# Kernel optimization log

Measured on AMD Instinct MI355X. Metric: run time of the kernel, lower is better.

Reference implementation:

```python
import jax, jax.numpy as jnp
import numpy as np

T, B, D, H, L = 512, 128, 256, 256, 4
EPS = 1e-5

def _ln(x, g, b):
    m = jnp.mean(x, axis=-1, keepdims=True)
    v = jnp.mean((x - m) ** 2, axis=-1, keepdims=True)
    return (x - m) * jax.lax.rsqrt(v + EPS) * g + b

def setup_inputs() -> dict:
    key = jax.random.key(0)
    ks = jax.random.split(key, 24)
    s = 0.02
    inp = {
        "x": jax.random.normal(ks[0], (T, B, D), dtype=jnp.float32),
        "lengths": jax.random.randint(ks[1], (B,), 1, T + 1, dtype=jnp.int32),
        # LinearEnchancedGRU params
        "Wr": jax.random.normal(ks[2], (D + H, H)) * s,
        "gr": jnp.ones((H,)), "br": jnp.zeros((H,)),
        "Wz": jax.random.normal(ks[3], (D + H, H)) * s,
        "gz": jnp.ones((H,)), "bz": jnp.zeros((H,)),
        "Wl": jax.random.normal(ks[4], (D + H, H)) * s,
        "gl": jnp.ones((H,)), "bl": jnp.zeros((H,)),
        "Wlt": jax.random.normal(ks[5], (D, H)) * s,
        "Cx": jax.random.normal(ks[6], (D, H)) * s,
        "Ch_w": jax.random.normal(ks[7], (H, H)) * s,
        "Ch_b": jnp.zeros((H,)),
        # TransitionGRU stack params [L, ...]
        "tWr": jax.random.normal(ks[8], (L, H, H)) * s,
        "tgr": jnp.ones((L, H)), "tbr": jnp.zeros((L, H)),
        "tWz": jax.random.normal(ks[9], (L, H, H)) * s,
        "tgz": jnp.ones((L, H)), "tbz": jnp.zeros((L, H)),
        "tWc": jax.random.normal(ks[10], (L, H, H)) * s,
        "tbc": jnp.zeros((L, H)),
    }
    return inp

def reference(x, lengths, Wr, gr, br, Wz, gz, bz, Wl, gl, bl, Wlt, Cx, Ch_w, Ch_b,
              tWr, tgr, tbr, tWz, tgz, tbz, tWc, tbc):
    # x: [T,B,D]; lengths: [B]. Packed-sequence semantics: hidden state of a
    # finished example is frozen; its outputs are zero padding.
    mask = jnp.arange(T, dtype=jnp.int32)[:, None] < lengths[None, :]  # [T,B]

    def cell(xt, h):
        cat = jnp.concatenate([xt, h], axis=-1)  # [B, D+H]
        r = jax.nn.sigmoid(_ln(cat @ Wr, gr, br))
        z = jax.nn.sigmoid(_ln(cat @ Wz, gz, bz))
        l = jax.nn.sigmoid(_ln(cat @ Wl, gl, bl))
        n = jnp.tanh(xt @ Cx + r * (h @ Ch_w + Ch_b)) + l * (xt @ Wlt)
        h = (1.0 - z) * h + z * n
        for i in range(L):  # deep transition stack (fixed small depth)
            ri = jax.nn.sigmoid(_ln(h @ tWr[i], tgr[i], tbr[i]))
            zi = jax.nn.sigmoid(_ln(h @ tWz[i], tgz[i], tbz[i]))
            ni = jnp.tanh(ri * (h @ tWc[i] + tbc[i]))
            h = (1.0 - zi) * ni + zi * h
        return h

    def step(h, inputs):
        xt, mt = inputs  # [B,D], [B]
        hn = cell(xt, h)
        hn = jnp.where(mt[:, None], hn, h)
        out = jnp.where(mt[:, None], hn, 0.0)
        return hn, out

    h0 = jnp.zeros((B, H), dtype=x.dtype)
    _, outs = jax.lax.scan(step, h0, (x, mask))  # outs: [T,B,H]
    return outs
```

## Files before the change

### kernel.cpp

```cpp
#include <hip/hip_runtime.h>
#include <hip/hip_bf16.h>

#define T_ 512
#define B_ 128
#define D_ 256
#define H_ 256
#define EPS 1e-5f

typedef __attribute__((ext_vector_type(8))) short short8;
typedef __attribute__((ext_vector_type(4))) short short4v;
typedef __attribute__((ext_vector_type(4))) float f32x4;

#define SLICE_E  86016
#define WT_TOTAL 1376256

#define STATS_OFFB 2752512UL
#define HX_OFFB    2850816UL
#define FLAG_OFFB  2981888UL
#define NFLAGS     512

#define L_XBF  0
#define L_HBF  8192
#define L_G6   16384
#define L_SRED 22528
#define L_AUX  23040
#define L_TRN  47616
#define L_END  145920

__device__ __forceinline__ short f2bf(float f) {
  unsigned u = __builtin_bit_cast(unsigned, f);
  u = (u + 0x7FFFu + ((u >> 16) & 1u)) >> 16;
  return (short)u;
}
__device__ __forceinline__ f32x4 zero4() { f32x4 z = {0.f, 0.f, 0.f, 0.f}; return z; }
__device__ __forceinline__ f32x4 mfma16(short8 a, short8 b, f32x4 c) {
  return __builtin_amdgcn_mfma_f32_16x16x32_bf16(a, b, c, 0, 0, 0);
}
__device__ __forceinline__ void waitv0() { asm volatile("s_waitcnt vmcnt(0)" ::: "memory"); }

__device__ __forceinline__ f32x4 ald4(float* p) {
  unsigned long long* q = (unsigned long long*)p;
  unsigned long long a = __hip_atomic_load(q,     __ATOMIC_RELAXED, __HIP_MEMORY_SCOPE_AGENT);
  unsigned long long b = __hip_atomic_load(q + 1, __ATOMIC_RELAXED, __HIP_MEMORY_SCOPE_AGENT);
  f32x4 v;
  v[0] = __builtin_bit_cast(float, (unsigned)(a & 0xffffffffu));
  v[1] = __builtin_bit_cast(float, (unsigned)(a >> 32));
  v[2] = __builtin_bit_cast(float, (unsigned)(b & 0xffffffffu));
  v[3] = __builtin_bit_cast(float, (unsigned)(b >> 32));
  return v;
}
__device__ __forceinline__ void ast1f(float* p, float v) {
  __hip_atomic_store((unsigned*)p, __builtin_bit_cast(unsigned, v),
                     __ATOMIC_RELAXED, __HIP_MEMORY_SCOPE_AGENT);
}

__global__ void prep_weights(const float* __restrict__ Wr, const float* __restrict__ Wz,
                             const float* __restrict__ Wl, const float* __restrict__ Wlt,
                             const float* __restrict__ Cx, const float* __restrict__ Chw,
                             const float* __restrict__ tWr, const float* __restrict__ tWz,
                             const float* __restrict__ tWc, short* __restrict__ wt) {
  int idx = blockIdx.x * 256 + threadIdx.x;
  if (idx >= WT_TOTAL) return;
  int j  = idx / SLICE_E;
  int r  = idx - j * SLICE_E;
  int u  = r >> 12;
  int rr = r & 4095;
  int kf = rr >> 9;
  int le = rr & 511;
  int l  = le >> 3, e = le & 7;
  int la = l & 15, lh = l >> 4;
  int col = j * 16 + la;
  float v;
  if (u < 6) {
    int g = u >> 1, half = u & 1;
    int k = half * 256 + lh * 8 + kf * 32 + e;
    const float* W = (g == 0) ? Wr : (g == 1 ? Wz : Wl);
    v = W[k * 256 + col];
  } else if (u < 9) {
    int a = u - 6;
    int k = lh * 8 + kf * 32 + e;
    const float* W = (a == 0) ? Cx : (a == 1 ? Wlt : Chw);
    v = W[k * 256 + col];
  } else {
    int q = u - 9;
    int li = q / 3, m = q - li * 3;
    int k = lh * 8 + kf * 32 + e;
    const float* W = (m == 0) ? tWr : (m == 1 ? tWz : tWc);
    v = W[(li * 256 + k) * 256 + col];
  }
  wt[idx] = f2bf(v);
}

__global__ __launch_bounds__(64)
void rnn_sx(const float* __restrict__ x, const int* __restrict__ lengths,
            const float* __restrict__ gr, const float* __restrict__ br,
            const float* __restrict__ gz, const float* __restrict__ bz,
            const float* __restrict__ gl, const float* __restrict__ bl,
            const float* __restrict__ Chb,
            const float* __restrict__ tgr, const float* __restrict__ tbr,
            const float* __restrict__ tgz, const float* __restrict__ tbz,
            const float* __restrict__ tbc,
            const short* __restrict__ W, float* __restrict__ stats,
            short* __restrict__ hxs, unsigned* __restrict__ flags,
            float* __restrict__ out) {

  __shared__ __align__(16) char smem[L_END];

  const int l  = threadIdx.x;
  const int la = l & 15, lh = l >> 4;
  const int amask = (la & 7) << 4;
  const int bid = blockIdx.x;
  const int cl = bid & 7, j = bid >> 3;
  const int rb0 = cl * 16;
  const int myrow = l >> 2, mc = (l & 3) * 4;
  const int cg = j * 16 + mc;
  const int colb = (l & 3) * 64;

  const short* Wsl = W + (size_t)j * SLICE_E;

  #pragma unroll 1
  for (int u = 0; u < 15; ++u) {
    char* dst = smem + ((u < 3) ? (L_AUX + u * 8192) : (L_TRN + (u - 3) * 8192));
    const short* src = Wsl + (size_t)(u + 6) * 4096;
    #pragma unroll
    for (int kf = 0; kf < 8; ++kf)
      *(short8*)(dst + kf * 1024 + l * 16) = *(const short8*)(src + kf * 512 + l * 8);
  }
  for (int i = l; i < 1024; i += 64) ((short4v*)(smem + L_HBF))[i] = (short4v){0, 0, 0, 0};

  int maxlen = 0;
  for (int i = 0; i < 16; ++i) {
    int v = lengths[rb0 + i];
    maxlen = maxlen > v ? maxlen : v;
  }
  const int mylen = lengths[rb0 + myrow];

  float* stc = stats + (size_t)(cl * 2) * 1536;
  short* hxc = hxs + (size_t)(cl * 2) * 4096;
  unsigned* flc = flags + cl * 64;

  f32x4 hreg = zero4();
  int dead = 0;

  auto pollf = [&](unsigned* fb, unsigned tag) {
    if (!dead) {
      int it = 0;
      while (true) {
        unsigned v = tag;
        if (l < 16) v = __hip_atomic_load(fb + l, __ATOMIC_RELAXED, __HIP_MEMORY_SCOPE_AGENT);
        if (__all((int)(v >= tag))) break;
        if (++it > 300000) { dead = 1; break; }
        __builtin_amdgcn_s_sleep(1);
      }
    }
    asm volatile("" ::: "memory");
  };
  auto ldu = [&](short8 (&dst)[8], const short* bp) {
    #pragma unroll
    for (int kf = 0; kf < 8; ++kf) dst[kf] = *(const short8*)(bp + kf * 512 + l * 8);
  };
  auto mm8r = [&](short8 (&Bv)[8], f32x4& acc, int Ab) {
    #pragma unroll
    for (int kf = 0; kf < 8; ++kf) {
      int aoff = Ab + la * 512 + (((kf * 64) + lh * 16) ^ amask);
      acc = mfma16(*(const short8*)(smem + aoff), Bv[kf], acc);
    }
  };
  auto mmlds = [&](int Bub, f32x4& acc, int Ab) {
    #pragma unroll
    for (int kf = 0; kf < 8; ++kf) {
      int aoff = Ab + la * 512 + (((kf * 64) + lh * 16) ^ amask);
      short8 bv = *(const short8*)(smem + Bub + kf * 1024 + l * 16);
      acc = mfma16(*(const short8*)(smem + aoff), bv, acc);
    }
  };
  auto g6store = [&](int arr, f32x4 acc) {
    #pragma unroll
    for (int i = 0; i < 4; ++i)
      *(float*)(smem + L_G6 + ((arr * 16 + lh * 4 + i) * 16 + la) * 4) = acc[i];
  };
  auto readhx = [&](int par) {
    float* hp = (float*)(hxc + par * 4096 + (l >> 2) * 256 + colb);
    int row2 = l >> 2;
    #pragma unroll
    for (int q2 = 0; q2 < 8; ++q2) {
      f32x4 v = ald4(hp + q2 * 4);
      *(f32x4*)(smem + L_HBF + row2 * 512 + ((colb * 2 + q2 * 16) ^ ((row2 & 7) << 4))) = v;
    }
  };
  auto posth = [&](int par) {
    unsigned long long pk =
        (unsigned long long)(unsigned short)f2bf(hreg[0]) |
        ((unsigned long long)(unsigned short)f2bf(hreg[1]) << 16) |
        ((unsigned long long)(unsigned short)f2bf(hreg[2]) << 32) |
        ((unsigned long long)(unsigned short)f2bf(hreg[3]) << 48);
    __hip_atomic_store((unsigned long long*)(hxc + par * 4096 + myrow * 256 + cg), pk,
                       __ATOMIC_RELAXED, __HIP_MEMORY_SCOPE_AGENT);
  };

  short8 B0[8], B1[8];
  ldu(B0, Wsl);
  ldu(B1, Wsl + 4096);

  for (int t = 0; t < maxlen; ++t) {
    int R = t * 5, par = R & 1;
    {
      const float* xs = x + ((size_t)t * B_ + rb0 + (l >> 2)) * D_ + colb;
      int row2 = l >> 2;
      #pragma unroll
      for (int u2 = 0; u2 < 8; ++u2) {
        f32x4 a = *(const f32x4*)(xs + u2 * 8);
        f32x4 b = *(const f32x4*)(xs + u2 * 8 + 4);
        short8 s;
        s[0] = f2bf(a[0]); s[1] = f2bf(a[1]); s[2] = f2bf(a[2]); s[3] = f2bf(a[3]);
        s[4] = f2bf(b[0]); s[5] = f2bf(b[1]); s[6] = f2bf(b[2]); s[7] = f2bf(b[3]);
        *(short8*)(smem + L_XBF + row2 * 512 + ((colb * 2 + u2 * 16) ^ ((row2 & 7) << 4))) = s;
      }
    }
    f32x4 ac[6];
    #pragma unroll
    for (int a2 = 0; a2 < 6; ++a2) ac[a2] = zero4();
    mm8r(B0, ac[0], L_XBF); ldu(B0, Wsl + 2 * 4096);
    mm8r(B1, ac[0], L_HBF); ldu(B1, Wsl + 3 * 4096);
    mm8r(B0, ac[1], L_XBF); ldu(B0, Wsl + 4 * 4096);
    mm8r(B1, ac[1], L_HBF); ldu(B1, Wsl + 5 * 4096);
    mm8r(B0, ac[2], L_XBF);
    mm8r(B1, ac[2], L_HBF);
    mmlds(L_AUX,         ac[3], L_XBF);
    mmlds(L_AUX + 8192,  ac[4], L_XBF);
    mmlds(L_AUX + 16384, ac[5], L_HBF);
    #pragma unroll
    for (int a2 = 0; a2 < 6; ++a2) g6store(a2, ac[a2]);
    f32x4 pv[6];
    #pragma unroll
    for (int a2 = 0; a2 < 6; ++a2)
      pv[a2] = *(const f32x4*)(smem + L_G6 + ((a2 * 16 + myrow) * 16 + mc) * 4);
    float st[6];
    #pragma unroll
    for (int g2 = 0; g2 < 3; ++g2) {
      f32x4 v = pv[g2];
      st[2 * g2]     = v[0] + v[1] + v[2] + v[3];
      st[2 * g2 + 1] = v[0] * v[0] + v[1] * v[1] + v[2] * v[2] + v[3] * v[3];
    }
    #pragma unroll
    for (int s2 = 0; s2 < 6; ++s2) {
      st[s2] += __shfl_xor(st[s2], 1);
      st[s2] += __shfl_xor(st[s2], 2);
    }
    float* sp = stc + par * 1536;
    {
      int k4 = l & 3;
      ast1f(sp + (k4 * 16 + myrow) * 16 + j, st[k4]);
      if (k4 < 2) ast1f(sp + ((4 + k4) * 16 + myrow) * 16 + j, st[4 + k4]);
    }
    waitv0();
    if (l == 0)
      __hip_atomic_store(flc + par * 16 + j, (unsigned)(R + 1),
                         __ATOMIC_RELAXED, __HIP_MEMORY_SCOPE_AGENT);
    pollf(flc + par * 16, (unsigned)(R + 1));
    {
      float* q = sp + l * 16;
      f32x4 a = ald4(q), b = ald4(q + 4), c = ald4(q + 8), d = ald4(q + 12);
      f32x4 s4 = a + b + c + d;
      *(float*)(smem + L_SRED + l * 4) = s4[0] + s4[1] + s4[2] + s4[3];
      if (l < 32) {
        float* q2 = sp + (64 + l) * 16;
        f32x4 a2 = ald4(q2), b2 = ald4(q2 + 4), c2 = ald4(q2 + 8), d2 = ald4(q2 + 12);
        f32x4 t4 = a2 + b2 + c2 + d2;
        *(float*)(smem + L_SRED + (64 + l) * 4) = t4[0] + t4[1] + t4[2] + t4[3];
      }
    }
    {
      float m3[3], rs3[3];
      #pragma unroll
      for (int g2 = 0; g2 < 3; ++g2) {
        float s1 = *(float*)(smem + L_SRED + ((2 * g2) * 16 + myrow) * 4);
        float s2 = *(float*)(smem + L_SRED + ((2 * g2 + 1) * 16 + myrow) * 4);
        float mm = s1 * (1.f / 256.f);
        float vv = s2 * (1.f / 256.f) - mm * mm;
        m3[g2] = mm; rs3[g2] = rsqrtf((vv > 0.f ? vv : 0.f) + EPS);
      }
      f32x4 g4r = *(const f32x4*)(gr + cg), b4r = *(const f32x4*)(br + cg);
      f32x4 g4z = *(const f32x4*)(gz + cg), b4z = *(const f32x4*)(bz + cg);
      f32x4 g4l = *(const f32x4*)(gl + cg), b4l = *(const f32x4*)(bl + cg);
      f32x4 cb4 = *(const f32x4*)(Chb + cg);
      bool act = t < mylen;
      f32x4 hn;
      #pragma unroll
      for (int q2 = 0; q2 < 4; ++q2) {
        float rv = 1.f / (1.f + __expf(-((pv[0][q2] - m3[0]) * rs3[0] * g4r[q2] + b4r[q2])));
        float zv = 1.f / (1.f + __expf(-((pv[1][q2] - m3[1]) * rs3[1] * g4z[q2] + b4z[q2])));
        float lv = 1.f / (1.f + __expf(-((pv[2][q2] - m3[2]) * rs3[2] * g4l[q2] + b4l[q2])));
        float n = tanhf(pv[3][q2] + rv * (pv[5][q2] + cb4[q2])) + lv * pv[4][q2];
        hn[q2] = (1.f - zv) * hreg[q2] + zv * n;
      }
      if (act) hreg = hn;
    }
    posth(par);
    waitv0();
    if (l == 0)
      __hip_atomic_store(flc + (2 + par) * 16 + j, (unsigned)(R + 1),
                         __ATOMIC_RELAXED, __HIP_MEMORY_SCOPE_AGENT);
    pollf(flc + (2 + par) * 16, (unsigned)(R + 1));
    readhx(par);

    #pragma unroll 1
    for (int li = 0; li < 4; ++li) {
      R = t * 5 + 1 + li; par = R & 1;
      f32x4 tc0 = zero4(), tc1 = zero4(), tc2 = zero4();
      mmlds(L_TRN + (li * 3 + 0) * 8192, tc0, L_HBF);
      mmlds(L_TRN + (li * 3 + 1) * 8192, tc1, L_HBF);
      mmlds(L_TRN + (li * 3 + 2) * 8192, tc2, L_HBF);
      g6store(0, tc0); g6store(1, tc1); g6store(2, tc2);
      f32x4 qv[3];
      #pragma unroll
      for (int a2 = 0; a2 < 3; ++a2)
        qv[a2] = *(const f32x4*)(smem + L_G6 + ((a2 * 16 + myrow) * 16 + mc) * 4);
      float st4[4];
      #pragma unroll
      for (int g2 = 0; g2 < 2; ++g2) {
        f32x4 v = qv[g2];
        st4[2 * g2]     = v[0] + v[1] + v[2] + v[3];
        st4[2 * g2 + 1] = v[0] * v[0] + v[1] * v[1] + v[2] * v[2] + v[3] * v[3];
      }
      #pragma unroll
      for (int s2 = 0; s2 < 4; ++s2) {
        st4[s2] += __shfl_xor(st4[s2], 1);
        st4[s2] += __shfl_xor(st4[s2], 2);
      }
      float* sp2 = stc + par * 1536;
      ast1f(sp2 + ((l & 3) * 16 + myrow) * 16 + j, st4[l & 3]);
      waitv0();
      if (l == 0)
        __hip_atomic_store(flc + par * 16 + j, (unsigned)(R + 1),
                           __ATOMIC_RELAXED, __HIP_MEMORY_SCOPE_AGENT);
      if (li == 3) {
        ldu(B0, Wsl);
        ldu(B1, Wsl + 4096);
      }
      pollf(flc + par * 16, (unsigned)(R + 1));
      {
        float* q = sp2 + l * 16;
        f32x4 a = ald4(q), b = ald4(q + 4), c = ald4(q + 8), d = ald4(q + 12);
        f32x4 s4 = a + b + c + d;
        *(float*)(smem + L_SRED + l * 4) = s4[0] + s4[1] + s4[2] + s4[3];
      }
      bool act = t < mylen;
      {
        float m2[2], rs2[2];
        #pragma unroll
        for (int g2 = 0; g2 < 2; ++g2) {
          float s1 = *(float*)(smem + L_SRED + ((2 * g2) * 16 + myrow) * 4);
          float s2 = *(float*)(smem + L_SRED + ((2 * g2 + 1) * 16 + myrow) * 4);
          float mm = s1 * (1.f / 256.f);
          float vv = s2 * (1.f / 256.f) - mm * mm;
          m2[g2] = mm; rs2[g2] = rsqrtf((vv > 0.f ? vv : 0.f) + EPS);
        }
        f32x4 g4r = *(const f32x4*)(tgr + li * 256 + cg), b4r = *(const f32x4*)(tbr + li * 256 + cg);
        f32x4 g4z = *(const f32x4*)(tgz + li * 256 + cg), b4z = *(const f32x4*)(tbz + li * 256 + cg);
        f32x4 cb4 = *(const f32x4*)(tbc + li * 256 + cg);
        f32x4 hn;
        #pragma unroll
        for (int q2 = 0; q2 < 4; ++q2) {
          float rv = 1.f / (1.f + __expf(-((qv[0][q2] - m2[0]) * rs2[0] * g4r[q2] + b4r[q2])));
          float zv = 1.f / (1.f + __expf(-((qv[1][q2] - m2[1]) * rs2[1] * g4z[q2] + b4z[q2])));
          float n = tanhf(rv * (qv[2][q2] + cb4[q2]));
          hn[q2] = (1.f - zv) * n + zv * hreg[q2];
        }
        if (act) hreg = hn;
        if (li == 3) {
          f32x4 o = act ? hreg : zero4();
          *(f32x4*)(out + ((size_t)t * B_ + rb0 + myrow) * H_ + cg) = o;
        }
      }
      posth(par);
      waitv0();
      if (l == 0)
        __hip_atomic_store(flc + (2 + par) * 16 + j, (unsigned)(R + 1),
                           __ATOMIC_RELAXED, __HIP_MEMORY_SCOPE_AGENT);
      pollf(flc + (2 + par) * 16, (unsigned)(R + 1));
      readhx(par);
    }
  }

  for (int t2 = maxlen; t2 < T_; ++t2)
    *(f32x4*)(out + ((size_t)t2 * B_ + rb0 + myrow) * H_ + cg) = zero4();
}

extern "C" void kernel_launch(void* const* d_in, const int* in_sizes, int n_in,
                              void* d_out, int out_size, void* d_ws, size_t ws_size,
                              hipStream_t stream) {
  const float* x    = (const float*)d_in[0];
  const int* lengths = (const int*)d_in[1];
  const float* Wr   = (const float*)d_in[2];
  const float* gr   = (const float*)d_in[3];
  const float* br   = (const float*)d_in[4];
  const float* Wz   = (const float*)d_in[5];
  const float* gz   = (const float*)d_in[6];
  const float* bz   = (const float*)d_in[7];
  const float* Wl   = (const float*)d_in[8];
  const float* gl   = (const float*)d_in[9];
  const float* bl   = (const float*)d_in[10];
  const float* Wlt  = (const float*)d_in[11];
  const float* Cx   = (const float*)d_in[12];
  const float* Chw  = (const float*)d_in[13];
  const float* Chb  = (const float*)d_in[14];
  const float* tWr  = (const float*)d_in[15];
  const float* tgr  = (const float*)d_in[16];
  const float* tbr  = (const float*)d_in[17];
  const float* tWz  = (const float*)d_in[18];
  const float* tgz  = (const float*)d_in[19];
  const float* tbz  = (const float*)d_in[20];
  const float* tWc  = (const float*)d_in[21];
  const float* tbc  = (const float*)d_in[22];

  short*    wt    = (short*)d_ws;
  float*    stats = (float*)((char*)d_ws + STATS_OFFB);
  short*    hxs   = (short*)((char*)d_ws + HX_OFFB);
  unsigned* flags = (unsigned*)((char*)d_ws + FLAG_OFFB);

  hipMemsetAsync(flags, 0, NFLAGS * sizeof(unsigned), stream);
  hipLaunchKernelGGL(prep_weights, dim3((WT_TOTAL + 255) / 256), dim3(256), 0, stream,
                     Wr, Wz, Wl, Wlt, Cx, Chw, tWr, tWz, tWc, wt);
  hipLaunchKernelGGL(rnn_sx, dim3(128), dim3(64), 0, stream,
                     x, lengths, gr, br, gz, bz, gl, bl, Chb,
                     tgr, tbr, tgz, tbz, tbc, wt, stats, hxs, flags, (float*)d_out);
}
```

Before: 17.77 ms.

## Embed step tags in hidden-state exchange words to drop the per-phase flag barrier

Each published bf16 hidden-state word now carries the round tag in its upper 32 bits, so readers spin directly on the data until all tags match. This removes the separate flag store, wait and poll that followed every h exchange, which was five per timestep. The flag poll is also changed to per-lane spinning with a short busy wait before sleeping. The cost is that the hidden-state buffer doubles in size, readers issue 32 atomic 8-byte loads per lane in each poll iteration, and correctness now rests on a per-word tag check instead of a store-then-flag ordering.

Result: no change. 17.89 ms (+0.7%).

```diff
diff --git a/kernel.cpp b/kernel.cpp
--- a/kernel.cpp
+++ b/kernel.cpp
@@ -10,14 +10,17 @@
 typedef __attribute__((ext_vector_type(8))) short short8;
 typedef __attribute__((ext_vector_type(4))) short short4v;
 typedef __attribute__((ext_vector_type(4))) float f32x4;
+typedef __attribute__((ext_vector_type(4))) unsigned u32x4;
+typedef unsigned long long ull;
 
 #define SLICE_E  86016
 #define WT_TOTAL 1376256
 
 #define STATS_OFFB 2752512UL
 #define HX_OFFB    2850816UL
-#define FLAG_OFFB  2981888UL
-#define NFLAGS     512
+#define FLAG_OFFB  3112960UL
+#define SYNC0_OFFB HX_OFFB
+#define SYNC0_BYTES (262144UL + 1024UL)
 
 #define L_XBF  0
 #define L_HBF  8192
@@ -39,9 +42,9 @@
 __device__ __forceinline__ void waitv0() { asm volatile("s_waitcnt vmcnt(0)" ::: "memory"); }
 
 __device__ __forceinline__ f32x4 ald4(float* p) {
-  unsigned long long* q = (unsigned long long*)p;
-  unsigned long long a = __hip_atomic_load(q,     __ATOMIC_RELAXED, __HIP_MEMORY_SCOPE_AGENT);
-  unsigned long long b = __hip_atomic_load(q + 1, __ATOMIC_RELAXED, __HIP_MEMORY_SCOPE_AGENT);
+  ull* q = (ull*)p;
+  ull a = __hip_atomic_load(q,     __ATOMIC_RELAXED, __HIP_MEMORY_SCOPE_AGENT);
+  ull b = __hip_atomic_load(q + 1, __ATOMIC_RELAXED, __HIP_MEMORY_SCOPE_AGENT);
   f32x4 v;
   v[0] = __builtin_bit_cast(float, (unsigned)(a & 0xffffffffu));
   v[1] = __builtin_bit_cast(float, (unsigned)(a >> 32));
@@ -52,6 +55,12 @@
 __device__ __forceinline__ void ast1f(float* p, float v) {
   __hip_atomic_store((unsigned*)p, __builtin_bit_cast(unsigned, v),
                      __ATOMIC_RELAXED, __HIP_MEMORY_SCOPE_AGENT);
+}
+__device__ __forceinline__ ull ald8(ull* p) {
+  return __hip_atomic_load(p, __ATOMIC_RELAXED, __HIP_MEMORY_SCOPE_AGENT);
+}
+__device__ __forceinline__ void ast8(ull* p, ull v) {
+  __hip_atomic_store(p, v, __ATOMIC_RELAXED, __HIP_MEMORY_SCOPE_AGENT);
 }
 
 __global__ void prep_weights(const float* __restrict__ Wr, const float* __restrict__ Wz,
@@ -101,7 +110,7 @@
             const float* __restrict__ tgz, const float* __restrict__ tbz,
             const float* __restrict__ tbc,
             const short* __restrict__ W, float* __restrict__ stats,
-            short* __restrict__ hxs, unsigned* __restrict__ flags,
+            ull* __restrict__ hx8, unsigned* __restrict__ flags,
             float* __restrict__ out) {
 
   __shared__ __align__(16) char smem[L_END];
@@ -136,21 +145,19 @@
   const int mylen = lengths[rb0 + myrow];
 
   float* stc = stats + (size_t)(cl * 2) * 1536;
-  short* hxc = hxs + (size_t)(cl * 2) * 4096;
-  unsigned* flc = flags + cl * 64;
+  ull*   hxc = hx8 + (size_t)cl * 4096;
+  unsigned* flc = flags + cl * 32;
 
   f32x4 hreg = zero4();
   int dead = 0;
 
-  auto pollf = [&](unsigned* fb, unsigned tag) {
-    if (!dead) {
+  auto pollf = [&](int par, unsigned tag) {
+    if (!dead && l < 16) {
+      unsigned* sp = flc + par * 16 + l;
       int it = 0;
-      while (true) {
-        unsigned v = tag;
-        if (l < 16) v = __hip_atomic_load(fb + l, __ATOMIC_RELAXED, __HIP_MEMORY_SCOPE_AGENT);
-        if (__all((int)(v >= tag))) break;
+      while (__hip_atomic_load(sp, __ATOMIC_RELAXED, __HIP_MEMORY_SCOPE_AGENT) < tag) {
         if (++it > 300000) { dead = 1; break; }
-        __builtin_amdgcn_s_sleep(1);
+        if (it > 4) __builtin_amdgcn_s_sleep(1);
       }
     }
     asm volatile("" ::: "memory");
@@ -179,23 +186,42 @@
     for (int i = 0; i < 4; ++i)
       *(float*)(smem + L_G6 + ((arr * 16 + lh * 4 + i) * 16 + la) * 4) = acc[i];
   };
-  auto readhx = [&](int par) {
-    float* hp = (float*)(hxc + par * 4096 + (l >> 2) * 256 + colb);
+  auto posth = [&](int par, unsigned tag) {
+    unsigned lo0 = (unsigned)(unsigned short)f2bf(hreg[0]) |
+                   ((unsigned)(unsigned short)f2bf(hreg[1]) << 16);
+    unsigned lo1 = (unsigned)(unsigned short)f2bf(hreg[2]) |
+                   ((unsigned)(unsigned short)f2bf(hreg[3]) << 16);
+    ull* hp = hxc + par * 2048 + myrow * 128 + j * 8 + (l & 3) * 2;
+    ast8(hp,     (ull)lo0 | ((ull)tag << 32));
+    ast8(hp + 1, (ull)lo1 | ((ull)tag << 32));
+  };
+  auto readhx = [&](int par, unsigned tag) {
     int row2 = l >> 2;
-    #pragma unroll
-    for (int q2 = 0; q2 < 8; ++q2) {
-      f32x4 v = ald4(hp + q2 * 4);
-      *(f32x4*)(smem + L_HBF + row2 * 512 + ((colb * 2 + q2 * 16) ^ ((row2 & 7) << 4))) = v;
-    }
-  };
-  auto posth = [&](int par) {
-    unsigned long long pk =
-        (unsigned long long)(unsigned short)f2bf(hreg[0]) |
-        ((unsigned long long)(unsigned short)f2bf(hreg[1]) << 16) |
-        ((unsigned long long)(unsigned short)f2bf(hreg[2]) << 32) |
-        ((unsigned long long)(unsigned short)f2bf(hreg[3]) << 48);
-    __hip_atomic_store((unsigned long long*)(hxc + par * 4096 + myrow * 256 + cg), pk,
-                       __ATOMIC_RELAXED, __HIP_MEMORY_SCOPE_AGENT);
+    ull* hp = hxc + par * 2048 + row2 * 128 + (l & 3) * 32;
+    unsigned lo[32];
+    bool ok = false;
+    int it = 0;
+    for (;;) {
+      if (!ok) {
+        unsigned mn = 0xffffffffu;
+        #pragma unroll
+        for (int k = 0; k < 32; ++k) {
+          ull v = ald8(hp + k);
+          lo[k] = (unsigned)v;
+          unsigned tg = (unsigned)(v >> 32);
+          mn = mn < tg ? mn : tg;
+        }
+        ok = (mn >= tag);
+      }
+      if (__all((int)ok) || dead) break;
+      if (++it > 100000) dead = 1;
+      if (it > 4) __builtin_amdgcn_s_sleep(1);
+    }
+    #pragma unroll
+    for (int q = 0; q < 8; ++q) {
+      u32x4 v = { lo[4 * q], lo[4 * q + 1], lo[4 * q + 2], lo[4 * q + 3] };
+      *(u32x4*)(smem + L_HBF + row2 * 512 + (((l & 3) * 128 + q * 16) ^ ((row2 & 7) << 4))) = v;
+    }
   };
 
   short8 B0[8], B1[8];
@@ -204,6 +230,7 @@
 
   for (int t = 0; t < maxlen; ++t) {
     int R = t * 5, par = R & 1;
+    unsigned tag = (unsigned)(R + 1);
     {
       const float* xs = x + ((size_t)t * B_ + rb0 + (l >> 2)) * D_ + colb;
       int row2 = l >> 2;
@@ -255,9 +282,8 @@
     }
     waitv0();
     if (l == 0)
-      __hip_atomic_store(flc + par * 16 + j, (unsigned)(R + 1),
-                         __ATOMIC_RELAXED, __HIP_MEMORY_SCOPE_AGENT);
-    pollf(flc + par * 16, (unsigned)(R + 1));
+      __hip_atomic_store(flc + par * 16 + j, tag, __ATOMIC_RELAXED, __HIP_MEMORY_SCOPE_AGENT);
+    pollf(par, tag);
     {
       float* q = sp + l * 16;
       f32x4 a = ald4(q), b = ald4(q + 4), c = ald4(q + 8), d = ald4(q + 12);
@@ -296,17 +322,12 @@
       }
       if (act) hreg = hn;
     }
-    posth(par);
-    waitv0();
-    if (l == 0)
-      __hip_atomic_store(flc + (2 + par) * 16 + j, (unsigned)(R + 1),
-                         __ATOMIC_RELAXED, __HIP_MEMORY_SCOPE_AGENT);
-    pollf(flc + (2 + par) * 16, (unsigned)(R + 1));
-    readhx(par);
+    posth(par, tag);
+    readhx(par, tag);
 
     #pragma unroll 1
     for (int li = 0; li < 4; ++li) {
-      R = t * 5 + 1 + li; par = R & 1;
+      R = t * 5 + 1 + li; par = R & 1; tag = (unsigned)(R + 1);
       f32x4 tc0 = zero4(), tc1 = zero4(), tc2 = zero4();
       mmlds(L_TRN + (li * 3 + 0) * 8192, tc0, L_HBF);
       mmlds(L_TRN + (li * 3 + 1) * 8192, tc1, L_HBF);
@@ -332,13 +353,12 @@
       ast1f(sp2 + ((l & 3) * 16 + myrow) * 16 + j, st4[l & 3]);
       waitv0();
       if (l == 0)
-        __hip_atomic_store(flc + par * 16 + j, (unsigned)(R + 1),
-                           __ATOMIC_RELAXED, __HIP_MEMORY_SCOPE_AGENT);
+        __hip_atomic_store(flc + par * 16 + j, tag, __ATOMIC_RELAXED, __HIP_MEMORY_SCOPE_AGENT);
       if (li == 3) {
         ldu(B0, Wsl);
         ldu(B1, Wsl + 4096);
       }
-      pollf(flc + par * 16, (unsigned)(R + 1));
+      pollf(par, tag);
       {
         float* q = sp2 + l * 16;
         f32x4 a = ald4(q), b = ald4(q + 4), c = ald4(q + 8), d = ald4(q + 12);
@@ -373,13 +393,8 @@
           *(f32x4*)(out + ((size_t)t * B_ + rb0 + myrow) * H_ + cg) = o;
         }
       }
-      posth(par);
-      waitv0();
-      if (l == 0)
-        __hip_atomic_store(flc + (2 + par) * 16 + j, (unsigned)(R + 1),
-                           __ATOMIC_RELAXED, __HIP_MEMORY_SCOPE_AGENT);
-      pollf(flc + (2 + par) * 16, (unsigned)(R + 1));
-      readhx(par);
+      posth(par, tag);
+      readhx(par, tag);
     }
   }
 
@@ -416,13 +431,13 @@
 
   short*    wt    = (short*)d_ws;
   float*    stats = (float*)((char*)d_ws + STATS_OFFB);
-  short*    hxs   = (short*)((char*)d_ws + HX_OFFB);
+  ull*      hx8   = (ull*)((char*)d_ws + HX_OFFB);
   unsigned* flags = (unsigned*)((char*)d_ws + FLAG_OFFB);
 
-  hipMemsetAsync(flags, 0, NFLAGS * sizeof(unsigned), stream);
+  hipMemsetAsync((char*)d_ws + SYNC0_OFFB, 0, SYNC0_BYTES, stream);
   hipLaunchKernelGGL(prep_weights, dim3((WT_TOTAL + 255) / 256), dim3(256), 0, stream,
                      Wr, Wz, Wl, Wlt, Cx, Chw, tWr, tWz, tWc, wt);
   hipLaunchKernelGGL(rnn_sx, dim3(128), dim3(64), 0, stream,
                      x, lengths, gr, br, gz, bz, gl, bl, Chb,
-                     tgr, tbr, tgz, tbz, tbc, wt, stats, hxs, flags, (float*)d_out);
-}
+                     tgr, tbr, tgz, tbz, tbc, wt, stats, hx8, flags, (float*)d_out);
+}
```
